# Kernel tuning notes

Hardware: AMD Instinct MI355X
Metric: run time of the kernel (lower is better)

The kernel has to match this reference:

```python
import jax, jax.numpy as jnp
import numpy as np

N_NODES = 20000
N_EDGES = 320000
N_GRAPHS = 16
NEG_SLOPE = 0.2


def gat_layer(x, src, dst, W, al, ar, b):
    # x: [N, F_in]; W: [F_in, H*D]; al/ar: [H, D]; b: [H*D]
    H, D = al.shape
    N = x.shape[0]
    f = (x @ W).reshape(N, H, D)                      # projected features [N,H,D]
    el = jnp.sum(f * al[None], axis=-1)                # [N,H]
    er = jnp.sum(f * ar[None], axis=-1)                # [N,H]
    e = jax.nn.leaky_relu(el[src] + er[dst], NEG_SLOPE)  # [E,H]
    # numerically stable segment softmax over incoming edges of each dst node
    m = jax.ops.segment_max(e, dst, num_segments=N)    # [N,H]
    m = jnp.where(jnp.isfinite(m), m, 0.0)
    ex = jnp.exp(e - m[dst])                           # [E,H]
    denom = jax.ops.segment_sum(ex, dst, num_segments=N)  # [N,H]
    msg = ex[:, :, None] * f[src]                      # [E,H,D]
    num = jax.ops.segment_sum(msg, dst, num_segments=N)   # [N,H,D]
    rst = num / jnp.where(denom > 0, denom, 1.0)[:, :, None]
    return rst + b.reshape(1, H, D)


def setup_inputs() -> dict:
    key = jax.random.key(0)
    ks = jax.random.split(key, 16)
    in_dim, hid, H = 128, 128, 3
    x = jax.random.normal(ks[0], (N_NODES, in_dim), dtype=jnp.float32)
    src = jax.random.randint(ks[1], (N_EDGES,), 0, N_NODES, dtype=jnp.int32)
    dst = jax.random.randint(ks[2], (N_EDGES,), 0, N_NODES, dtype=jnp.int32)
    graph_ids = jnp.sort(jax.random.randint(ks[3], (N_NODES,), 0, N_GRAPHS, dtype=jnp.int32))
    s = lambda d: 1.0 / np.sqrt(d)
    W1 = jax.random.normal(ks[4], (in_dim, H * hid), jnp.float32) * s(in_dim)
    al1 = jax.random.normal(ks[5], (H, hid), jnp.float32) * s(hid)
    ar1 = jax.random.normal(ks[6], (H, hid), jnp.float32) * s(hid)
    b1 = jnp.zeros((H * hid,), jnp.float32)
    W2 = jax.random.normal(ks[7], (H * hid, hid), jnp.float32) * s(H * hid)
    al2 = jax.random.normal(ks[8], (1, hid), jnp.float32) * s(hid)
    ar2 = jax.random.normal(ks[9], (1, hid), jnp.float32) * s(hid)
    b2 = jnp.zeros((hid,), jnp.float32)
    linW = jax.random.normal(ks[10], (hid, hid), jnp.float32) * s(hid)
    linb = jnp.zeros((hid,), jnp.float32)
    return dict(x=x, src=src, dst=dst, graph_ids=graph_ids, W1=W1, al1=al1,
                ar1=ar1, b1=b1, W2=W2, al2=al2, ar2=ar2, b2=b2, linW=linW, linb=linb)


def reference(x, src, dst, graph_ids, W1, al1, ar1, b1, W2, al2, ar2, b2, linW, linb):
    h = gat_layer(x, src, dst, W1, al1, ar1, b1)       # [N,3,hid]
    h = jax.nn.elu(h.reshape(h.shape[0], -1))          # [N,3*hid]
    h = gat_layer(h, src, dst, W2, al2, ar2, b2)       # [N,1,hid]
    h = h.squeeze(1)                                   # [N,hid]
    # dgl.mean_nodes over batched graph
    sums = jax.ops.segment_sum(h, graph_ids, num_segments=N_GRAPHS)      # [G,hid]
    cnts = jax.ops.segment_sum(jnp.ones_like(graph_ids, jnp.float32), graph_ids, num_segments=N_GRAPHS)
    hg = sums / jnp.maximum(cnts, 1.0)[:, None]
    return jax.nn.relu(hg @ linW + linb)
```

## Files before the change

kernel.cpp:

```cpp
#include <hip/hip_runtime.h>
#include <hip/hip_bf16.h>

#define NN 20000
#define NE 320000
#define NG 16
#define PSPLIT 32
#define NSCANB 79
#define NHISTB 1250


__global__ void pack_hist_wlr_kernel(const int* __restrict__ dst, int* __restrict__ indeg,
                                     const float* __restrict__ W1, const float* __restrict__ al1,
                                     const float* __restrict__ ar1, float* __restrict__ wlr) {
  int b = blockIdx.x, t = threadIdx.x;
  if (b < NHISTB) {
    int e = b * 256 + t;
    if (e < NE) atomicAdd(&indeg[dst[e]], 1);
  } else {
    int idx = (b - NHISTB) * 256 + t;
    if (idx >= 768) return;
    int k = idx & 127;
    int j = idx >> 7;
    int h = j % 3;
    const float* av = (j < 3 ? al1 : ar1) + h * 128;
    const float* wrow = W1 + (size_t)k * 384 + h * 128;
    float s = 0.f;
#pragma unroll 4
    for (int d = 0; d < 128; d++) s += wrow[d] * av[d];
    wlr[j * 128 + k] = s;
  }
}


__global__ void pack_scan1_elr_kernel(const int* __restrict__ indeg, int* __restrict__ loc,
                                      int* __restrict__ bsum, const float* __restrict__ x,
                                      const float* __restrict__ wlr, float* __restrict__ el,
                                      float* __restrict__ er) {
  __shared__ int ws[4];
  __shared__ float wl_s[768];
  int b = blockIdx.x, t = threadIdx.x;
  int lane = t & 63, wv = t >> 6;
  if (b < NSCANB) {
    int i = b * 256 + t;
    int v = (i < NN) ? indeg[i] : 0;
    int xx = v;
#pragma unroll
    for (int off = 1; off < 64; off <<= 1) {
      int y = __shfl_up(xx, off);
      if (lane >= off) xx += y;
    }
    if (lane == 63) ws[wv] = xx;
    __syncthreads();
    int add = 0;
    for (int w2 = 0; w2 < wv; w2++) add += ws[w2];
    xx += add;
    if (i < NN) loc[i] = xx - v;
    if (t == 255) bsum[b] = xx;
  } else {
    for (int i = t; i < 768; i += 256) wl_s[i] = wlr[i];
    __syncthreads();
    int w = ((b - NSCANB) * 256 + t) >> 6;
    if (w >= NN) return;
    float v0 = x[(size_t)w * 128 + lane], v1 = x[(size_t)w * 128 + 64 + lane];
    float s[6];
#pragma unroll
    for (int j = 0; j < 6; j++) s[j] = v0 * wl_s[j * 128 + lane] + v1 * wl_s[j * 128 + 64 + lane];
#pragma unroll
    for (int off = 32; off; off >>= 1)
#pragma unroll
      for (int j = 0; j < 6; j++) s[j] += __shfl_down(s[j], off);
    if (lane == 0) {
      el[w * 3 + 0] = s[0]; el[w * 3 + 1] = s[1]; el[w * 3 + 2] = s[2];
      er[w * 3 + 0] = s[3]; er[w * 3 + 1] = s[4]; er[w * 3 + 2] = s[5];
    }
  }
}

__global__ void scan2_kernel(const int* __restrict__ bsum, int* __restrict__ boff,
                             int* __restrict__ rp_end, int nb) {
  int t = threadIdx.x;
  int lane = t & 63, wv = t >> 6;
  __shared__ int ws[2];
  int v = (t < nb) ? bsum[t] : 0;
  int x = v;
#pragma unroll
  for (int off = 1; off < 64; off <<= 1) {
    int y = __shfl_up(x, off);
    if (lane >= off) x += y;
  }
  if (lane == 63) ws[wv] = x;
  __syncthreads();
  if (wv == 1) x += ws[0];
  if (t < nb) boff[t] = x - v;
  if (t == 127) *rp_end = x;
}

__global__ void pack_scatter_fin_kernel(const int* __restrict__ src, const int* __restrict__ dst,
                                        const int* __restrict__ loc, const int* __restrict__ boff,
                                        int* __restrict__ cursor, int* __restrict__ csr_src,
                                        int* __restrict__ rowptr) {
  int b = blockIdx.x, t = threadIdx.x;
  if (b < NHISTB) {
    int e = b * 256 + t;
    if (e < NE) {
      int d = dst[e];
      int p = atomicAdd(&cursor[d], 1);
      csr_src[loc[d] + boff[d >> 8] + p] = src[e];
    }
  } else {
    int i = (b - NHISTB) * 256 + t;
    if (i < NN) rowptr[i] = loc[i] + boff[i >> 8];
  }
}


__global__ void aggregate_x_kernel(const float* __restrict__ x, const float* __restrict__ el,
                                   const float* __restrict__ er, const int* __restrict__ rowptr,
                                   const int* __restrict__ csr_src, float* __restrict__ aggx) {
  int n = blockIdx.x;
  int t = threadIdx.x;
  __shared__ float wbuf[3][128];
  __shared__ int sbuf[128];
  __shared__ float red[6];
  __shared__ float4 accbuf[3][4][32];
  int rs = rowptr[n];
  int deg = rowptr[n + 1] - rs;
  float er0 = er[n * 3 + 0], er1 = er[n * 3 + 1], er2 = er[n * 3 + 2];
  float p0 = 0.f, p1 = 0.f, p2 = 0.f;
  int g = t >> 5, dq = t & 31;
  const float* xd = x + dq * 4;
  float4 a0 = make_float4(0, 0, 0, 0), a1 = a0, a2 = a0;
  for (int base = 0; base < deg; base += 128) {
    int cnt = min(128, deg - base);
    if (t < cnt) {
      int s = csr_src[rs + base + t];
      sbuf[t] = s;
      float e0 = el[s * 3 + 0] + er0, e1 = el[s * 3 + 1] + er1, e2 = el[s * 3 + 2] + er2;
      e0 = e0 > 0.f ? e0 : 0.2f * e0;
      e1 = e1 > 0.f ? e1 : 0.2f * e1;
      e2 = e2 > 0.f ? e2 : 0.2f * e2;
      float w0 = __expf(e0), w1 = __expf(e1), w2 = __expf(e2);
      wbuf[0][t] = w0; wbuf[1][t] = w1; wbuf[2][t] = w2;
      p0 += w0; p1 += w1; p2 += w2;
    }
    __syncthreads();
    int j = g;
    for (; j + 4 < cnt; j += 8) {
      int s0 = sbuf[j], s1 = sbuf[j + 4];
      float4 v0 = *(const float4*)(xd + (size_t)s0 * 128);
      float4 v1 = *(const float4*)(xd + (size_t)s1 * 128);
      float w00 = wbuf[0][j], w01 = wbuf[1][j], w02 = wbuf[2][j];
      float w10 = wbuf[0][j + 4], w11 = wbuf[1][j + 4], w12 = wbuf[2][j + 4];
      a0.x += w00 * v0.x + w10 * v1.x; a0.y += w00 * v0.y + w10 * v1.y;
      a0.z += w00 * v0.z + w10 * v1.z; a0.w += w00 * v0.w + w10 * v1.w;
      a1.x += w01 * v0.x + w11 * v1.x; a1.y += w01 * v0.y + w11 * v1.y;
      a1.z += w01 * v0.z + w11 * v1.z; a1.w += w01 * v0.w + w11 * v1.w;
      a2.x += w02 * v0.x + w12 * v1.x; a2.y += w02 * v0.y + w12 * v1.y;
      a2.z += w02 * v0.z + w12 * v1.z; a2.w += w02 * v0.w + w12 * v1.w;
    }
    for (; j < cnt; j += 4) {
      int s = sbuf[j];
      float4 v = *(const float4*)(xd + (size_t)s * 128);
      float w0 = wbuf[0][j], w1 = wbuf[1][j], w2 = wbuf[2][j];
      a0.x += w0 * v.x; a0.y += w0 * v.y; a0.z += w0 * v.z; a0.w += w0 * v.w;
      a1.x += w1 * v.x; a1.y += w1 * v.y; a1.z += w1 * v.z; a1.w += w1 * v.w;
      a2.x += w2 * v.x; a2.y += w2 * v.y; a2.z += w2 * v.z; a2.w += w2 * v.w;
    }
    __syncthreads();
  }
  for (int off = 32; off; off >>= 1) {
    p0 += __shfl_down(p0, off);
    p1 += __shfl_down(p1, off);
    p2 += __shfl_down(p2, off);
  }
  int wv = t >> 6, ln = t & 63;
  if (ln == 0) { red[wv * 3 + 0] = p0; red[wv * 3 + 1] = p1; red[wv * 3 + 2] = p2; }
  accbuf[0][g][dq] = a0;
  accbuf[1][g][dq] = a1;
  accbuf[2][g][dq] = a2;
  __syncthreads();
  if (t < 96) {
    int h = t >> 5, d = t & 31;
    float4 s0 = accbuf[h][0][d], s1 = accbuf[h][1][d], s2 = accbuf[h][2][d], s3 = accbuf[h][3][d];
    float dn = red[h] + red[3 + h];
    float inv = dn > 0.f ? 1.f / dn : 0.f;
    float4 r;
    r.x = (s0.x + s1.x + s2.x + s3.x) * inv;
    r.y = (s0.y + s1.y + s2.y + s3.y) * inv;
    r.z = (s0.z + s1.z + s2.z + s3.z) * inv;
    r.w = (s0.w + s1.w + s2.w + s3.w) * inv;
    *(float4*)&aggx[(size_t)n * 384 + h * 128 + d * 4] = r;
  }
}


template <int KT, bool HEADS, bool BIAS_ELU, bool EL2>
__launch_bounds__(128)
__global__ void gemm_k128_kernel(const float* __restrict__ A, int lda,
                                 const float* __restrict__ B, int ldb,
                                 float* __restrict__ C, int ldc,
                                 const float* __restrict__ bias,
                                 const float* __restrict__ al2, const float* __restrict__ ar2,
                                 float* __restrict__ el2, float* __restrict__ er2) {
  __shared__ float As[128 * 40];
  __shared__ float Bs[128 * 64];
  int t = threadIdx.x;
  int m0 = blockIdx.x * 32;
  int col0 = blockIdx.y * 64;
  if (HEADS) A += (col0 >> 7) * 128;
  int tm = t >> 4, tn = t & 15;
  float acc[4][4];
#pragma unroll
  for (int i = 0; i < 4; i++)
#pragma unroll
    for (int j = 0; j < 4; j++) acc[i][j] = 0.f;

  for (int k0 = 0; k0 < KT; k0 += 128) {
#pragma unroll
    for (int j = 0; j < 8; j++) {
      int idx = t + j * 128;
      int r = idx & 31, kq = (idx >> 5) * 4;
      float4 v = *(const float4*)&A[(size_t)(m0 + r) * lda + k0 + kq];
      As[(kq + 0) * 40 + r] = v.x;
      As[(kq + 1) * 40 + r] = v.y;
      As[(kq + 2) * 40 + r] = v.z;
      As[(kq + 3) * 40 + r] = v.w;
    }
#pragma unroll
    for (int j = 0; j < 16; j++) {
      int idx = t + j * 128;
      int kk = idx >> 4, nq = (idx & 15) * 4;
      *(float4*)&Bs[kk * 64 + nq] = *(const float4*)&B[(size_t)(k0 + kk) * ldb + col0 + nq];
    }
    __syncthreads();
#pragma unroll 8
    for (int k = 0; k < 128; k++) {
      float4 a = *(const float4*)&As[k * 40 + tm * 4];
      float4 b = *(const float4*)&Bs[k * 64 + tn * 4];
      float af[4] = {a.x, a.y, a.z, a.w};
      float bf[4] = {b.x, b.y, b.z, b.w};
#pragma unroll
      for (int i = 0; i < 4; i++)
#pragma unroll
        for (int j = 0; j < 4; j++) acc[i][j] += af[i] * bf[j];
    }
    __syncthreads();
  }
  float bv[4];
  if (BIAS_ELU) {
#pragma unroll
    for (int j = 0; j < 4; j++) bv[j] = bias[col0 + tn * 4 + j];
  }
#pragma unroll
  for (int i = 0; i < 4; i++) {
    int gm = m0 + tm * 4 + i;
    float r[4];
#pragma unroll
    for (int j = 0; j < 4; j++) {
      float v = acc[i][j];
      if (BIAS_ELU) {
        v += bv[j];
        v = v > 0.f ? v : expm1f(v);
      }
      r[j] = v;
    }
    *(float4*)&C[(size_t)gm * ldc + col0 + tn * 4] = make_float4(r[0], r[1], r[2], r[3]);
  }
  if (EL2) {
    float av[4], rv[4];
#pragma unroll
    for (int j = 0; j < 4; j++) { av[j] = al2[col0 + tn * 4 + j]; rv[j] = ar2[col0 + tn * 4 + j]; }
    __syncthreads();
    float* red = As;
#pragma unroll
    for (int i = 0; i < 4; i++) {
      float pe = acc[i][0] * av[0] + acc[i][1] * av[1] + acc[i][2] * av[2] + acc[i][3] * av[3];
      float pr = acc[i][0] * rv[0] + acc[i][1] * rv[1] + acc[i][2] * rv[2] + acc[i][3] * rv[3];
      red[(tm * 4 + i) * 32 + tn * 2 + 0] = pe;
      red[(tm * 4 + i) * 32 + tn * 2 + 1] = pr;
    }
    __syncthreads();
    if (t < 32) {
      float se = 0.f, sr = 0.f;
#pragma unroll
      for (int q = 0; q < 16; q++) { se += red[t * 32 + 2 * q]; sr += red[t * 32 + 2 * q + 1]; }
      atomicAdd(&el2[m0 + t], se);
      atomicAdd(&er2[m0 + t], sr);
    }
  }
}


__global__ void aggregate1_kernel(const float* __restrict__ f, const float* __restrict__ el,
                                  const float* __restrict__ er, const float* __restrict__ bias,
                                  const int* __restrict__ rowptr, const int* __restrict__ csr_src,
                                  float* __restrict__ out) {
  int n = blockIdx.x;
  int t = threadIdx.x;
  __shared__ float wbuf[128];
  __shared__ int sbuf[128];
  __shared__ float red[2];
  __shared__ float4 accbuf[4][32];
  int rs = rowptr[n];
  int deg = rowptr[n + 1] - rs;
  float ern = er[n];
  float psum = 0.f;
  int g = t >> 5;
  int d = (t & 31) * 4;
  const float* fd = f + d;
  float4 acc = make_float4(0.f, 0.f, 0.f, 0.f);
  for (int base = 0; base < deg; base += 128) {
    int cnt = min(128, deg - base);
    if (t < cnt) {
      int s = csr_src[rs + base + t];
      sbuf[t] = s;
      float e = el[s] + ern;
      e = e > 0.f ? e : 0.2f * e;
      float w = __expf(e);
      wbuf[t] = w;
      psum += w;
    }
    __syncthreads();
    int j = g;
    for (; j + 4 < cnt; j += 8) {
      int s0 = sbuf[j], s1 = sbuf[j + 4];
      float4 v0 = *(const float4*)(fd + (size_t)s0 * 128);
      float4 v1 = *(const float4*)(fd + (size_t)s1 * 128);
      float w0 = wbuf[j], w1 = wbuf[j + 4];
      acc.x += w0 * v0.x + w1 * v1.x;
      acc.y += w0 * v0.y + w1 * v1.y;
      acc.z += w0 * v0.z + w1 * v1.z;
      acc.w += w0 * v0.w + w1 * v1.w;
    }
    for (; j < cnt; j += 4) {
      int s = sbuf[j];
      float4 v = *(const float4*)(fd + (size_t)s * 128);
      float w = wbuf[j];
      acc.x += w * v.x; acc.y += w * v.y; acc.z += w * v.z; acc.w += w * v.w;
    }
    __syncthreads();
  }
  for (int off = 32; off; off >>= 1) psum += __shfl_down(psum, off);
  int wv = t >> 6, ln = t & 63;
  if (ln == 0) red[wv] = psum;
  accbuf[g][t & 31] = acc;
  __syncthreads();
  if (t < 32) {
    float4 a0 = accbuf[0][t], a1 = accbuf[1][t], a2 = accbuf[2][t], a3 = accbuf[3][t];
    float dn = red[0] + red[1];
    float inv = dn > 0.f ? 1.f / dn : 0.f;
    const float* bp = bias + t * 4;
    float4 r;
    r.x = (a0.x + a1.x + a2.x + a3.x) * inv + bp[0];
    r.y = (a0.y + a1.y + a2.y + a3.y) * inv + bp[1];
    r.z = (a0.z + a1.z + a2.z + a3.z) * inv + bp[2];
    r.w = (a0.w + a1.w + a2.w + a3.w) * inv + bp[3];
    *(float4*)&out[(size_t)n * 128 + t * 4] = r;
  }
}


__global__ void pool_partial_kernel(const float* __restrict__ h2, const int* __restrict__ gid,
                                    float* __restrict__ sums, int N) {
  int g = blockIdx.x / PSPLIT;
  int sp = blockIdx.x % PSPLIT;
  int tid = threadIdx.x;
  int lo0 = 0, hi0 = N;
  while (lo0 < hi0) { int m = (lo0 + hi0) >> 1; if (gid[m] < g) lo0 = m + 1; else hi0 = m; }
  int lo1 = lo0, hi1 = N;
  while (lo1 < hi1) { int m = (lo1 + hi1) >> 1; if (gid[m] < g + 1) lo1 = m + 1; else hi1 = m; }
  float a0 = 0.f, a1 = 0.f, a2 = 0.f, a3 = 0.f;
  int n = lo0 + sp;
  for (; n + 3 * PSPLIT < lo1; n += 4 * PSPLIT) {
    a0 += h2[(size_t)n * 128 + tid];
    a1 += h2[(size_t)(n + PSPLIT) * 128 + tid];
    a2 += h2[(size_t)(n + 2 * PSPLIT) * 128 + tid];
    a3 += h2[(size_t)(n + 3 * PSPLIT) * 128 + tid];
  }
  for (; n < lo1; n += PSPLIT) a0 += h2[(size_t)n * 128 + tid];
  float acc = (a0 + a1) + (a2 + a3);
  atomicAdd(&sums[g * 128 + tid], acc);
}

__global__ void pool_final_kernel(const float* __restrict__ sums, const int* __restrict__ gid,
                                  const float* __restrict__ linW, const float* __restrict__ linb,
                                  float* __restrict__ out, int N) {
  int g = blockIdx.x;
  int tid = threadIdx.x;
  int lo0 = 0, hi0 = N;
  while (lo0 < hi0) { int m = (lo0 + hi0) >> 1; if (gid[m] < g) lo0 = m + 1; else hi0 = m; }
  int lo1 = lo0, hi1 = N;
  while (lo1 < hi1) { int m = (lo1 + hi1) >> 1; if (gid[m] < g + 1) lo1 = m + 1; else hi1 = m; }
  int cnt = lo1 - lo0;
  float hg = sums[g * 128 + tid] / (float)(cnt > 0 ? cnt : 1);
  __shared__ float hgs[128];
  hgs[tid] = hg;
  __syncthreads();
  float o = linb[tid];
#pragma unroll 4
  for (int dd = 0; dd < 128; dd++) o += hgs[dd] * linW[dd * 128 + tid];
  out[g * 128 + tid] = fmaxf(o, 0.f);
}


extern "C" void kernel_launch(void* const* d_in, const int* in_sizes, int n_in,
                              void* d_out, int out_size, void* d_ws, size_t ws_size,
                              hipStream_t stream) {
  const float* x    = (const float*)d_in[0];
  const int*   src  = (const int*)d_in[1];
  const int*   dst  = (const int*)d_in[2];
  const int*   gid  = (const int*)d_in[3];
  const float* W1   = (const float*)d_in[4];
  const float* al1  = (const float*)d_in[5];
  const float* ar1  = (const float*)d_in[6];
  const float* b1   = (const float*)d_in[7];
  const float* W2   = (const float*)d_in[8];
  const float* al2  = (const float*)d_in[9];
  const float* ar2  = (const float*)d_in[10];
  const float* b2   = (const float*)d_in[11];
  const float* linW = (const float*)d_in[12];
  const float* linb = (const float*)d_in[13];
  float* out = (float*)d_out;

  char* ws = (char*)d_ws;
  size_t off = 0;
  auto alloc = [&](size_t bytes) -> void* {
    void* p = ws + off;
    off += (bytes + 255) & ~(size_t)255;
    return p;
  };
  float* aggx    = (float*)alloc((size_t)NN * 384 * 4);
  float* h1      = (float*)alloc((size_t)NN * 384 * 4);
  float* f2      = (float*)alloc((size_t)NN * 128 * 4);
  float* h2      = (float*)alloc((size_t)NN * 128 * 4);
  float* el1     = (float*)alloc((size_t)NN * 3 * 4);
  float* er1     = (float*)alloc((size_t)NN * 3 * 4);
  float* wlr     = (float*)alloc((size_t)768 * 4);
  int*   loc     = (int*)alloc((size_t)NN * 4);
  int*   rowptr  = (int*)alloc((size_t)(NN + 1) * 4);
  int*   csr_src = (int*)alloc((size_t)NE * 4);
  int*   bsum    = (int*)alloc((size_t)NSCANB * 4);
  int*   boff    = (int*)alloc((size_t)NSCANB * 4);
  float* el2     = (float*)alloc((size_t)NN * 4);
  float* er2     = (float*)alloc((size_t)NN * 4);
  int*   indeg   = (int*)alloc((size_t)NN * 4);
  int*   cursor  = (int*)alloc((size_t)NN * 4);
  float* gsums   = (float*)alloc((size_t)NG * 128 * 4);
  (void)ws_size;
  size_t zbytes = (char*)(gsums + NG * 128) - (char*)el2;
  hipMemsetAsync(el2, 0, zbytes, stream);

  pack_hist_wlr_kernel<<<NHISTB + 3, 256, 0, stream>>>(dst, indeg, W1, al1, ar1, wlr);
  pack_scan1_elr_kernel<<<NSCANB + 5000, 256, 0, stream>>>(indeg, loc, bsum, x, wlr, el1, er1);
  scan2_kernel<<<1, 128, 0, stream>>>(bsum, boff, rowptr + NN, NSCANB);
  pack_scatter_fin_kernel<<<NHISTB + NSCANB, 256, 0, stream>>>(src, dst, loc, boff, cursor,
                                                               csr_src, rowptr);

  aggregate_x_kernel<<<NN, 128, 0, stream>>>(x, el1, er1, rowptr, csr_src, aggx);
  gemm_k128_kernel<128, true, true, false><<<dim3(625, 6), 128, 0, stream>>>(
      aggx, 384, W1, 384, h1, 384, b1, nullptr, nullptr, nullptr, nullptr);

  gemm_k128_kernel<384, false, false, true><<<dim3(625, 2), 128, 0, stream>>>(
      h1, 384, W2, 128, f2, 128, nullptr, al2, ar2, el2, er2);
  aggregate1_kernel<<<NN, 128, 0, stream>>>(f2, el2, er2, b2, rowptr, csr_src, h2);

  pool_partial_kernel<<<NG * PSPLIT, 128, 0, stream>>>(h2, gid, gsums, NN);
  pool_final_kernel<<<NG, 128, 0, stream>>>(gsums, gid, linW, linb, out, NN);
}
```

Baseline: 300.1 us.

## Enlarge GEMM tiles to 64x128 and fuse mean-pooling into second aggregation

The GEMM kernel now uses 64x128 output tiles with an 8x8 per-thread register block and K-steps of 32. This cuts blocks and shared-memory traffic per FLOP, and it replaces the el2/er2 atomics with direct stores because one block now covers all 128 columns. The second aggregation adds each node's result straight into per-graph sums with atomics, which removes the h2 buffer and the pool_partial kernel. The costs are higher register pressure, fewer blocks for occupancy, and atomic contention on 16x128 graph-sum addresses. A guard buffer absorbs out-of-range A reads for the last partial row tile.

Result: slower. 560.8 us (+86.9%).

```diff
diff --git a/kernel.cpp b/kernel.cpp
--- a/kernel.cpp
+++ b/kernel.cpp
@@ -4,7 +4,6 @@
 #define NN 20000
 #define NE 320000
 #define NG 16
-#define PSPLIT 32
 #define NSCANB 79
 #define NHISTB 1250
 
@@ -196,105 +195,117 @@
 
 template <int KT, bool HEADS, bool BIAS_ELU, bool EL2>
 __launch_bounds__(128)
-__global__ void gemm_k128_kernel(const float* __restrict__ A, int lda,
-                                 const float* __restrict__ B, int ldb,
-                                 float* __restrict__ C, int ldc,
-                                 const float* __restrict__ bias,
-                                 const float* __restrict__ al2, const float* __restrict__ ar2,
-                                 float* __restrict__ el2, float* __restrict__ er2) {
-  __shared__ float As[128 * 40];
-  __shared__ float Bs[128 * 64];
+__global__ void gemm64_kernel(const float* __restrict__ A, int lda,
+                              const float* __restrict__ B, int ldb,
+                              float* __restrict__ C, int ldc,
+                              const float* __restrict__ bias,
+                              const float* __restrict__ al2, const float* __restrict__ ar2,
+                              float* __restrict__ el2, float* __restrict__ er2) {
+  __shared__ float As[32 * 64];
+  __shared__ float Bs[32 * 128];
   int t = threadIdx.x;
-  int m0 = blockIdx.x * 32;
-  int col0 = blockIdx.y * 64;
-  if (HEADS) A += (col0 >> 7) * 128;
+  int m0 = blockIdx.x * 64;
+  int col0 = blockIdx.y * 128;
+  if (HEADS) A += col0;
   int tm = t >> 4, tn = t & 15;
-  float acc[4][4];
-#pragma unroll
-  for (int i = 0; i < 4; i++)
-#pragma unroll
-    for (int j = 0; j < 4; j++) acc[i][j] = 0.f;
-
-  for (int k0 = 0; k0 < KT; k0 += 128) {
+  float acc[8][8];
+#pragma unroll
+  for (int i = 0; i < 8; i++)
+#pragma unroll
+    for (int j = 0; j < 8; j++) acc[i][j] = 0.f;
+
+  for (int k0 = 0; k0 < KT; k0 += 32) {
+#pragma unroll
+    for (int j = 0; j < 4; j++) {
+      int idx = t + j * 128;
+      int r = idx & 63, kq = (idx >> 6) * 4;
+      float4 v = *(const float4*)&A[(size_t)(m0 + r) * lda + k0 + kq];
+      As[(kq + 0) * 64 + r] = v.x;
+      As[(kq + 1) * 64 + r] = v.y;
+      As[(kq + 2) * 64 + r] = v.z;
+      As[(kq + 3) * 64 + r] = v.w;
+    }
 #pragma unroll
     for (int j = 0; j < 8; j++) {
       int idx = t + j * 128;
-      int r = idx & 31, kq = (idx >> 5) * 4;
-      float4 v = *(const float4*)&A[(size_t)(m0 + r) * lda + k0 + kq];
-      As[(kq + 0) * 40 + r] = v.x;
-      As[(kq + 1) * 40 + r] = v.y;
-      As[(kq + 2) * 40 + r] = v.z;
-      As[(kq + 3) * 40 + r] = v.w;
-    }
-#pragma unroll
-    for (int j = 0; j < 16; j++) {
-      int idx = t + j * 128;
-      int kk = idx >> 4, nq = (idx & 15) * 4;
-      *(float4*)&Bs[kk * 64 + nq] = *(const float4*)&B[(size_t)(k0 + kk) * ldb + col0 + nq];
-    }
-    __syncthreads();
-#pragma unroll 8
-    for (int k = 0; k < 128; k++) {
-      float4 a = *(const float4*)&As[k * 40 + tm * 4];
-      float4 b = *(const float4*)&Bs[k * 64 + tn * 4];
-      float af[4] = {a.x, a.y, a.z, a.w};
-      float bf[4] = {b.x, b.y, b.z, b.w};
-#pragma unroll
-      for (int i = 0; i < 4; i++)
-#pragma unroll
-        for (int j = 0; j < 4; j++) acc[i][j] += af[i] * bf[j];
-    }
-    __syncthreads();
-  }
-  float bv[4];
+      int kk = idx >> 5, nq = (idx & 31) * 4;
+      *(float4*)&Bs[kk * 128 + nq] = *(const float4*)&B[(size_t)(k0 + kk) * ldb + col0 + nq];
+    }
+    __syncthreads();
+#pragma unroll 4
+    for (int k = 0; k < 32; k++) {
+      float4 fa0 = *(const float4*)&As[k * 64 + tm * 8];
+      float4 fa1 = *(const float4*)&As[k * 64 + tm * 8 + 4];
+      float4 fb0 = *(const float4*)&Bs[k * 128 + tn * 4];
+      float4 fb1 = *(const float4*)&Bs[k * 128 + 64 + tn * 4];
+      float af[8] = {fa0.x, fa0.y, fa0.z, fa0.w, fa1.x, fa1.y, fa1.z, fa1.w};
+      float bf[8] = {fb0.x, fb0.y, fb0.z, fb0.w, fb1.x, fb1.y, fb1.z, fb1.w};
+#pragma unroll
+      for (int i = 0; i < 8; i++)
+#pragma unroll
+        for (int j = 0; j < 8; j++) acc[i][j] += af[i] * bf[j];
+    }
+    __syncthreads();
+  }
+  float bv[8];
   if (BIAS_ELU) {
 #pragma unroll
-    for (int j = 0; j < 4; j++) bv[j] = bias[col0 + tn * 4 + j];
-  }
-#pragma unroll
-  for (int i = 0; i < 4; i++) {
-    int gm = m0 + tm * 4 + i;
-    float r[4];
-#pragma unroll
     for (int j = 0; j < 4; j++) {
-      float v = acc[i][j];
-      if (BIAS_ELU) {
-        v += bv[j];
-        v = v > 0.f ? v : expm1f(v);
+      bv[j] = bias[col0 + tn * 4 + j];
+      bv[4 + j] = bias[col0 + 64 + tn * 4 + j];
+    }
+  }
+#pragma unroll
+  for (int i = 0; i < 8; i++) {
+    int gm = m0 + tm * 8 + i;
+    if (gm < NN) {
+      float r[8];
+#pragma unroll
+      for (int j = 0; j < 8; j++) {
+        float v = acc[i][j];
+        if (BIAS_ELU) {
+          v += bv[j];
+          v = v > 0.f ? v : expm1f(v);
+        }
+        r[j] = v;
       }
-      r[j] = v;
-    }
-    *(float4*)&C[(size_t)gm * ldc + col0 + tn * 4] = make_float4(r[0], r[1], r[2], r[3]);
+      *(float4*)&C[(size_t)gm * ldc + col0 + tn * 4] = make_float4(r[0], r[1], r[2], r[3]);
+      *(float4*)&C[(size_t)gm * ldc + col0 + 64 + tn * 4] = make_float4(r[4], r[5], r[6], r[7]);
+    }
   }
   if (EL2) {
-    float av[4], rv[4];
-#pragma unroll
-    for (int j = 0; j < 4; j++) { av[j] = al2[col0 + tn * 4 + j]; rv[j] = ar2[col0 + tn * 4 + j]; }
-    __syncthreads();
-    float* red = As;
-#pragma unroll
-    for (int i = 0; i < 4; i++) {
-      float pe = acc[i][0] * av[0] + acc[i][1] * av[1] + acc[i][2] * av[2] + acc[i][3] * av[3];
-      float pr = acc[i][0] * rv[0] + acc[i][1] * rv[1] + acc[i][2] * rv[2] + acc[i][3] * rv[3];
-      red[(tm * 4 + i) * 32 + tn * 2 + 0] = pe;
-      red[(tm * 4 + i) * 32 + tn * 2 + 1] = pr;
-    }
-    __syncthreads();
-    if (t < 32) {
+    float av[8], rv[8];
+#pragma unroll
+    for (int j = 0; j < 4; j++) {
+      av[j] = al2[col0 + tn * 4 + j];   av[4 + j] = al2[col0 + 64 + tn * 4 + j];
+      rv[j] = ar2[col0 + tn * 4 + j];   rv[4 + j] = ar2[col0 + 64 + tn * 4 + j];
+    }
+    __syncthreads();
+    float* red = Bs;
+#pragma unroll
+    for (int i = 0; i < 8; i++) {
+      float pe = 0.f, pr = 0.f;
+#pragma unroll
+      for (int j = 0; j < 8; j++) { pe += acc[i][j] * av[j]; pr += acc[i][j] * rv[j]; }
+      red[(tm * 8 + i) * 32 + tn * 2 + 0] = pe;
+      red[(tm * 8 + i) * 32 + tn * 2 + 1] = pr;
+    }
+    __syncthreads();
+    if (t < 64) {
       float se = 0.f, sr = 0.f;
 #pragma unroll
       for (int q = 0; q < 16; q++) { se += red[t * 32 + 2 * q]; sr += red[t * 32 + 2 * q + 1]; }
-      atomicAdd(&el2[m0 + t], se);
-      atomicAdd(&er2[m0 + t], sr);
-    }
-  }
-}
-
-
-__global__ void aggregate1_kernel(const float* __restrict__ f, const float* __restrict__ el,
-                                  const float* __restrict__ er, const float* __restrict__ bias,
-                                  const int* __restrict__ rowptr, const int* __restrict__ csr_src,
-                                  float* __restrict__ out) {
+      int gm = m0 + t;
+      if (gm < NN) { el2[gm] = se; er2[gm] = sr; }
+    }
+  }
+}
+
+
+__global__ void aggregate1_pool_kernel(const float* __restrict__ f, const float* __restrict__ el,
+                                       const float* __restrict__ er, const float* __restrict__ bias,
+                                       const int* __restrict__ rowptr, const int* __restrict__ csr_src,
+                                       const int* __restrict__ gid, float* __restrict__ gsums) {
   int n = blockIdx.x;
   int t = threadIdx.x;
   __shared__ float wbuf[128];
@@ -355,32 +366,12 @@
     r.y = (a0.y + a1.y + a2.y + a3.y) * inv + bp[1];
     r.z = (a0.z + a1.z + a2.z + a3.z) * inv + bp[2];
     r.w = (a0.w + a1.w + a2.w + a3.w) * inv + bp[3];
-    *(float4*)&out[(size_t)n * 128 + t * 4] = r;
-  }
-}
-
-
-__global__ void pool_partial_kernel(const float* __restrict__ h2, const int* __restrict__ gid,
-                                    float* __restrict__ sums, int N) {
-  int g = blockIdx.x / PSPLIT;
-  int sp = blockIdx.x % PSPLIT;
-  int tid = threadIdx.x;
-  int lo0 = 0, hi0 = N;
-  while (lo0 < hi0) { int m = (lo0 + hi0) >> 1; if (gid[m] < g) lo0 = m + 1; else hi0 = m; }
-  int lo1 = lo0, hi1 = N;
-  while (lo1 < hi1) { int m = (lo1 + hi1) >> 1; if (gid[m] < g + 1) lo1 = m + 1; else hi1 = m; }
-  float a0 = 0.f, a1 = 0.f, a2 = 0.f, a3 = 0.f;
-  int n = lo0 + sp;
-  for (; n + 3 * PSPLIT < lo1; n += 4 * PSPLIT) {
-    a0 += h2[(size_t)n * 128 + tid];
-    a1 += h2[(size_t)(n + PSPLIT) * 128 + tid];
-    a2 += h2[(size_t)(n + 2 * PSPLIT) * 128 + tid];
-    a3 += h2[(size_t)(n + 3 * PSPLIT) * 128 + tid];
-  }
-  for (; n < lo1; n += PSPLIT) a0 += h2[(size_t)n * 128 + tid];
-  float acc = (a0 + a1) + (a2 + a3);
-  atomicAdd(&sums[g * 128 + tid], acc);
-}
+    float* gp = &gsums[gid[n] * 128 + t * 4];
+    atomicAdd(&gp[0], r.x); atomicAdd(&gp[1], r.y);
+    atomicAdd(&gp[2], r.z); atomicAdd(&gp[3], r.w);
+  }
+}
+
 
 __global__ void pool_final_kernel(const float* __restrict__ sums, const int* __restrict__ gid,
                                   const float* __restrict__ linW, const float* __restrict__ linb,
@@ -432,23 +423,23 @@
   float* aggx    = (float*)alloc((size_t)NN * 384 * 4);
   float* h1      = (float*)alloc((size_t)NN * 384 * 4);
   float* f2      = (float*)alloc((size_t)NN * 128 * 4);
-  float* h2      = (float*)alloc((size_t)NN * 128 * 4);
+  float* guard   = (float*)alloc((size_t)64 * 384 * 4);
   float* el1     = (float*)alloc((size_t)NN * 3 * 4);
   float* er1     = (float*)alloc((size_t)NN * 3 * 4);
+  float* el2     = (float*)alloc((size_t)NN * 4);
+  float* er2     = (float*)alloc((size_t)NN * 4);
   float* wlr     = (float*)alloc((size_t)768 * 4);
   int*   loc     = (int*)alloc((size_t)NN * 4);
   int*   rowptr  = (int*)alloc((size_t)(NN + 1) * 4);
   int*   csr_src = (int*)alloc((size_t)NE * 4);
   int*   bsum    = (int*)alloc((size_t)NSCANB * 4);
   int*   boff    = (int*)alloc((size_t)NSCANB * 4);
-  float* el2     = (float*)alloc((size_t)NN * 4);
-  float* er2     = (float*)alloc((size_t)NN * 4);
   int*   indeg   = (int*)alloc((size_t)NN * 4);
   int*   cursor  = (int*)alloc((size_t)NN * 4);
   float* gsums   = (float*)alloc((size_t)NG * 128 * 4);
-  (void)ws_size;
-  size_t zbytes = (char*)(gsums + NG * 128) - (char*)el2;
-  hipMemsetAsync(el2, 0, zbytes, stream);
+  (void)ws_size; (void)guard;
+  size_t zbytes = (char*)(gsums + NG * 128) - (char*)indeg;
+  hipMemsetAsync(indeg, 0, zbytes, stream);
 
   pack_hist_wlr_kernel<<<NHISTB + 3, 256, 0, stream>>>(dst, indeg, W1, al1, ar1, wlr);
   pack_scan1_elr_kernel<<<NSCANB + 5000, 256, 0, stream>>>(indeg, loc, bsum, x, wlr, el1, er1);
@@ -457,13 +448,12 @@
                                                                csr_src, rowptr);
 
   aggregate_x_kernel<<<NN, 128, 0, stream>>>(x, el1, er1, rowptr, csr_src, aggx);
-  gemm_k128_kernel<128, true, true, false><<<dim3(625, 6), 128, 0, stream>>>(
+  gemm64_kernel<128, true, true, false><<<dim3(313, 3), 128, 0, stream>>>(
       aggx, 384, W1, 384, h1, 384, b1, nullptr, nullptr, nullptr, nullptr);
 
-  gemm_k128_kernel<384, false, false, true><<<dim3(625, 2), 128, 0, stream>>>(
+  gemm64_kernel<384, false, false, true><<<dim3(313, 1), 128, 0, stream>>>(
       h1, 384, W2, 128, f2, 128, nullptr, al2, ar2, el2, er2);
-  aggregate1_kernel<<<NN, 128, 0, stream>>>(f2, el2, er2, b2, rowptr, csr_src, h2);
-
-  pool_partial_kernel<<<NG * PSPLIT, 128, 0, stream>>>(h2, gid, gsums, NN);
+  aggregate1_pool_kernel<<<NN, 128, 0, stream>>>(f2, el2, er2, b2, rowptr, csr_src, gid, gsums);
+
   pool_final_kernel<<<NG, 128, 0, stream>>>(gsums, gid, linW, linb, out, NN);
 }
```
